# Kernel tuning notes

Hardware: AMD Instinct MI355X
Metric: run time of the kernel (lower is better)

## Reference

```python
import jax, jax.numpy as jnp
import numpy as np

B, LAT, NF, IMG, N_CALLS = 8, 512, 64, 128, 4
N_LAYERS = int(np.ceil(np.log2(IMG) - np.log2(16))) + 1  # 4 resolutions: 16,32,64,128
CF = 3  # SinSobel perception factor: identity + sobel_x + sobel_y
FIN, FH, FOUT = NF * CF, NF, NF * 2  # gated => 2*n_filter out of dyna block
P_SIZES = [FH * FIN, FH, FOUT * FH, FOUT, FOUT * FIN, FOUT]
P_OFFS = np.cumsum([0] + P_SIZES)
P_TOT = int(P_OFFS[-1])

_g1 = np.exp(-0.5 * np.array([-1.0, 0.0, 1.0]) ** 2)
_gk = np.outer(_g1, _g1); _gk = _gk / _gk.sum()
GAUSS_K = jnp.asarray(_gk, jnp.float32)
SOBEL_X = jnp.asarray(np.array([[-1, 0, 1], [-2, 0, 2], [-1, 0, 1]], np.float32) / 8.0)
SOBEL_Y = SOBEL_X.T


def _dwconv3(x, k):
    # depthwise 3x3 conv, 'same' padding; x: [B,C,H,W], k: [3,3]
    C = x.shape[1]
    kern = jnp.broadcast_to(k[None, None], (C, 1, 3, 3)).astype(x.dtype)
    return jax.lax.conv_general_dilated(
        x, kern, (1, 1), ((1, 1), (1, 1)),
        dimension_numbers=('NCHW', 'OIHW', 'NCHW'), feature_group_count=C)


def sin_sobel(x):
    # perception: [x, sobel_x(x), sobel_y(x)] -> 3*C channels
    return jnp.concatenate([x, _dwconv3(x, SOBEL_X), _dwconv3(x, SOBEL_Y)], axis=1)


def inst_norm(x, eps=1e-5):
    m = x.mean((2, 3), keepdims=True)
    v = x.var((2, 3), keepdims=True)
    return (x - m) * jax.lax.rsqrt(v + eps)


def up2_blur(x, gk):
    b, c, h, w = x.shape
    x = jax.image.resize(x, (b, c, 2 * h, 2 * w), 'bilinear')  # align_corners=False
    return _dwconv3(x, gk)


def dyna_block(x, lat, hyper_w, hyper_b):
    # hypernetwork generates per-sample 1x1-conv residual block weights
    p = lat @ hyper_w + hyper_b  # [B, P_TOT]
    w1 = p[:, P_OFFS[0]:P_OFFS[1]].reshape(-1, FH, FIN)
    b1 = p[:, P_OFFS[1]:P_OFFS[2]]
    w2 = p[:, P_OFFS[2]:P_OFFS[3]].reshape(-1, FOUT, FH)
    b2 = p[:, P_OFFS[3]:P_OFFS[4]]
    ws = p[:, P_OFFS[4]:P_OFFS[5]].reshape(-1, FOUT, FIN)
    bs = p[:, P_OFFS[5]:P_OFFS[6]]
    h = jax.nn.relu(jnp.einsum('bihw,boi->bohw', x, w1) + b1[:, :, None, None])
    y = jnp.einsum('bihw,boi->bohw', h, w2) + b2[:, :, None, None]
    s = jnp.einsum('bihw,boi->bohw', x, ws) + bs[:, :, None, None]
    return s + y


def setup_inputs() -> dict:
    key = jax.random.key(0)
    ks = jax.random.split(key, 8)
    return dict(
        lat=jax.random.normal(ks[0], (B, LAT), jnp.float32),
        ca_noise=jax.random.normal(ks[1], (B, NF, 16, 16), jnp.float32),
        seed=jax.random.normal(ks[2], (1, NF, 1, 1), jnp.float32),  # spatially constant seed
        leak_factor=jnp.asarray(0.1, jnp.float32),
        hyper_w=jax.random.normal(ks[3], (LAT, P_TOT), jnp.float32) * 0.02,
        hyper_b=jnp.zeros((P_TOT,), jnp.float32),
        res1_w=jax.random.normal(ks[4], (NF, NF), jnp.float32) / np.sqrt(NF).astype(np.float32),
        res1_b=jnp.zeros((NF,), jnp.float32),
        res2_w=jax.random.normal(ks[5], (NF, NF), jnp.float32) / np.sqrt(NF).astype(np.float32),
        res2_b=jnp.zeros((NF,), jnp.float32),
        outc_w=jax.random.normal(ks[6], (3, NF), jnp.float32) / np.sqrt(NF).astype(np.float32),
        outc_b=jnp.zeros((3,), jnp.float32),
    )


def reference(lat, ca_noise, seed, leak_factor, hyper_w, hyper_b,
              res1_w, res1_b, res2_w, res2_b, outc_w, outc_b):
    # seed init branch: constant seed -> instance_norm -> 0, plus blurred ca_noise
    out = inst_norm(jnp.broadcast_to(seed, (B, NF, 16, 16)))
    out = out + _dwconv3(ca_noise, GAUSS_K)  # in_ds (resize 16->16 is identity)
    lf = jnp.clip(leak_factor, 0.001, 1000.0)
    for c in range(N_LAYERS * N_CALLS):
        z = sin_sobel(out)
        z = inst_norm(z)
        z = dyna_block(z, lat, hyper_w, hyper_b)
        z, g = jnp.split(z, 2, axis=1)  # gated
        z = z * jax.nn.sigmoid(g)
        out = out + lf * z
        if c < N_LAYERS * N_CALLS - 1 and c % N_CALLS == N_CALLS - 1:
            out = up2_blur(out, GAUSS_K)
    # out_conv: resize to IMG is identity here; 1x1 residual block + 1x1 conv
    h = jax.nn.relu(jnp.einsum('bihw,oi->bohw', out, res1_w) + res1_b[None, :, None, None])
    r = jnp.einsum('bihw,oi->bohw', h, res2_w) + res2_b[None, :, None, None]
    y = jnp.einsum('bihw,oi->bohw', out + r, outc_w) + outc_b[None, :, None, None]
    out_raw = y
    return jnp.clip(y, -1.0, 1.0), out_raw
```

## Files before the change

kernel.cpp:

```cpp
#include <hip/hip_runtime.h>
#include <math.h>

#define B 8
#define LATD 512
#define PT 45376
#define FIN 192
#define FH 64
#define OW1 0
#define OB1 12288
#define OW2 12352
#define OB2 20544
#define OWS 20672
#define OBS 45248
#define TPX 128
#define KC 16

__device__ __forceinline__ float gk_at(int ky, int kx){
  const float a = 0.60653065971263342f;
  const float inv = 1.0f / ((1.0f + 2.0f*a) * (1.0f + 2.0f*a));
  float wy = (ky==1) ? 1.0f : a;
  float wx = (kx==1) ? 1.0f : a;
  return wy * wx * inv;
}

__global__ void k_hyper(const float* __restrict__ lat, const float* __restrict__ hw,
                        const float* __restrict__ hb, float* __restrict__ p){
  __shared__ float slat[B*LATD];
  for (int idx = threadIdx.x; idx < B*LATD; idx += 256) slat[idx] = lat[idx];
  __syncthreads();
  int j = blockIdx.x*256 + threadIdx.x;
  if (j >= PT) return;
  float acc[B];
#pragma unroll
  for (int b=0;b<B;++b) acc[b]=0.f;
  for (int k=0;k<LATD;++k){
    float w = hw[(size_t)k*PT + j];
#pragma unroll
    for (int b=0;b<B;++b) acc[b] = fmaf(slat[b*LATD+k], w, acc[b]);
  }
  float bias = hb[j];
#pragma unroll
  for (int b=0;b<B;++b) p[(size_t)b*PT + j] = acc[b] + bias;
}

__global__ void k_init(const float* __restrict__ noise, float* __restrict__ out){
  int bc = blockIdx.x;
  int t = threadIdx.x;
  int y = t >> 4, x = t & 15;
  const float* src = noise + (size_t)bc*256;
  float acc = 0.f;
#pragma unroll
  for (int ky=0;ky<3;++ky){
    int yy = y+ky-1; if (yy < 0 || yy > 15) continue;
#pragma unroll
    for (int kx=0;kx<3;++kx){
      int xx = x+kx-1; if (xx < 0 || xx > 15) continue;
      acc = fmaf(gk_at(ky,kx), src[yy*16+xx], acc);
    }
  }
  out[(size_t)bc*256 + t] = acc;
}

__global__ void __launch_bounds__(256) k_sobstat(const float* __restrict__ out, float* __restrict__ sob,
                    float* __restrict__ stats, int H, int lgH, int HW){
  int bc = blockIdx.x; int b = bc >> 6, c = bc & 63;
  int t = threadIdx.x;
  const float* src = out + ((size_t)(b*64+c))*(size_t)HW;
  float* dxp = sob + ((size_t)(b*128 + c))*(size_t)HW;
  float* dyp = sob + ((size_t)(b*128 + 64 + c))*(size_t)HW;
  float s0=0.f,q0=0.f,sx=0.f,qx=0.f,sy=0.f,qy=0.f;
  for (int px = t*4; px < HW; px += 1024){
    int y = px >> lgH, x = px & (H-1);
    float rm[6], rc[6], rp[6];
    float4 v = *(const float4*)(src + px);
    rc[1]=v.x; rc[2]=v.y; rc[3]=v.z; rc[4]=v.w;
    rc[0] = (x>0)     ? src[px-1] : 0.f;
    rc[5] = (x+4 < H) ? src[px+4] : 0.f;
    s0 += v.x+v.y+v.z+v.w;
    q0 += v.x*v.x+v.y*v.y+v.z*v.z+v.w*v.w;
    if (y > 0){
      const float* r = src + px - H;
      float4 u = *(const float4*)r;
      rm[1]=u.x; rm[2]=u.y; rm[3]=u.z; rm[4]=u.w;
      rm[0] = (x>0)     ? r[-1] : 0.f;
      rm[5] = (x+4 < H) ? r[4]  : 0.f;
    } else { rm[0]=rm[1]=rm[2]=rm[3]=rm[4]=rm[5]=0.f; }
    if (y+1 < H){
      const float* r = src + px + H;
      float4 u = *(const float4*)r;
      rp[1]=u.x; rp[2]=u.y; rp[3]=u.z; rp[4]=u.w;
      rp[0] = (x>0)     ? r[-1] : 0.f;
      rp[5] = (x+4 < H) ? r[4]  : 0.f;
    } else { rp[0]=rp[1]=rp[2]=rp[3]=rp[4]=rp[5]=0.f; }
    float dxv[4], dyv[4];
#pragma unroll
    for (int j=0;j<4;++j){
      dxv[j] = ((rm[j+2]-rm[j]) + 2.f*(rc[j+2]-rc[j]) + (rp[j+2]-rp[j])) * 0.125f;
      dyv[j] = ((rp[j] + 2.f*rp[j+1] + rp[j+2]) - (rm[j] + 2.f*rm[j+1] + rm[j+2])) * 0.125f;
      sx += dxv[j]; qx = fmaf(dxv[j],dxv[j],qx);
      sy += dyv[j]; qy = fmaf(dyv[j],dyv[j],qy);
    }
    float4 o1; o1.x=dxv[0]; o1.y=dxv[1]; o1.z=dxv[2]; o1.w=dxv[3];
    float4 o2; o2.x=dyv[0]; o2.y=dyv[1]; o2.z=dyv[2]; o2.w=dyv[3];
    *(float4*)(dxp + px) = o1;
    *(float4*)(dyp + px) = o2;
  }
  float vals[6] = {s0,q0,sx,qx,sy,qy};
  __shared__ float rbuf[6][4];
  int lane = t & 63, wid = t >> 6;
#pragma unroll
  for (int i=0;i<6;++i){
    float v = vals[i];
#pragma unroll
    for (int off=32; off; off>>=1) v += __shfl_down(v, off, 64);
    if (lane==0) rbuf[i][wid] = v;
  }
  __syncthreads();
  if (t < 3){
    float s = rbuf[t*2][0]+rbuf[t*2][1]+rbuf[t*2][2]+rbuf[t*2][3];
    float q = rbuf[t*2+1][0]+rbuf[t*2+1][1]+rbuf[t*2+1][2]+rbuf[t*2+1][3];
    float inv = 1.0f/(float)HW;
    float m = s*inv;
    float var = fmaxf(q*inv - m*m, 0.f);
    float r = 1.0f/sqrtf(var + 1e-5f);
    int ch = b*192 + c + t*64;
    stats[ch*2]   = -m*r;
    stats[ch*2+1] = r;
  }
}

__device__ __forceinline__ float4 ldx(const float* __restrict__ out, const float* __restrict__ sob,
                                      const float* __restrict__ stats,
                                      int b, int i, int off, int HW){
  const float* src = (i < 64) ? out + ((size_t)(b*64+i))*(size_t)HW
                              : sob + ((size_t)(b*128+(i-64)))*(size_t)HW;
  float4 v = *(const float4*)(src + off);
  float c = stats[(b*192+i)*2], r = stats[(b*192+i)*2+1];
  v.x = fmaf(v.x, r, c); v.y = fmaf(v.y, r, c);
  v.z = fmaf(v.z, r, c); v.w = fmaf(v.w, r, c);
  return v;
}

#define XS(k,p)  bufA[(k)*128 + (p)]
#define W1S(k,o) bufA[2048 + (k)*68 + (o)]
#define HS(k,p)  bufA[(k)*128 + (p)]
#define WZS(k,o) bufB[(k)*128 + (o)]
__global__ void __launch_bounds__(256, 3) k_dyna(float* __restrict__ out, const float* __restrict__ sob,
                       const float* __restrict__ stats, const float* __restrict__ p,
                       const float* __restrict__ lfp, int HW){
  __shared__ float bufA[8192];
  __shared__ float bufB[2048];
  int b = blockIdx.y;
  int tx = threadIdx.x, ty = threadIdx.y;
  int tid = ty*16 + tx;
  int px0 = blockIdx.x*TPX;
  const float* pw = p + (size_t)b*PT;

  float az[4][8], ag[4][8], ah[4][8];
#pragma unroll
  for (int k=0;k<4;++k)
#pragma unroll
    for (int j=0;j<8;++j){ az[k][j]=0.f; ag[k][j]=0.f; ah[k][j]=0.f; }

  const int xch0 = tid>>5,        xc4 = tid&31;
  const int xch1 = 8 + (tid>>5);
  const int wo0  = tid>>2,        wk  = tid&3;
  const int wo1  = 64 + (tid>>2);

  float4 vx0, vx1, vz0, vz1, v10;

  vx0 = ldx(out, sob, stats, b, xch0, px0 + xc4*4, HW);
  vx1 = ldx(out, sob, stats, b, xch1, px0 + xc4*4, HW);
  vz0 = *(const float4*)(pw + OWS + wo0*FIN + wk*4);
  vz1 = *(const float4*)(pw + OWS + wo1*FIN + wk*4);
  v10 = *(const float4*)(pw + OW1 + wo0*FIN + wk*4);

  for (int ci=0; ci<12; ++ci){
    __syncthreads();
    *(float4*)(&XS(xch0, xc4*4)) = vx0;
    *(float4*)(&XS(xch1, xc4*4)) = vx1;
    WZS(wk*4+0,wo0)=vz0.x; WZS(wk*4+1,wo0)=vz0.y; WZS(wk*4+2,wo0)=vz0.z; WZS(wk*4+3,wo0)=vz0.w;
    WZS(wk*4+0,wo1)=vz1.x; WZS(wk*4+1,wo1)=vz1.y; WZS(wk*4+2,wo1)=vz1.z; WZS(wk*4+3,wo1)=vz1.w;
    W1S(wk*4+0,wo0)=v10.x; W1S(wk*4+1,wo0)=v10.y; W1S(wk*4+2,wo0)=v10.z; W1S(wk*4+3,wo0)=v10.w;
    if (ci+1 < 12){
      int cn = ci+1;
      vx0 = ldx(out, sob, stats, b, cn*KC+xch0, px0 + xc4*4, HW);
      vx1 = ldx(out, sob, stats, b, cn*KC+xch1, px0 + xc4*4, HW);
      vz0 = *(const float4*)(pw + OWS + wo0*FIN + cn*KC + wk*4);
      vz1 = *(const float4*)(pw + OWS + wo1*FIN + cn*KC + wk*4);
      v10 = *(const float4*)(pw + OW1 + wo0*FIN + cn*KC + wk*4);
    }
    __syncthreads();
#pragma unroll 4
    for (int kk=0; kk<KC; ++kk){
      float4 xa = *(const float4*)(&XS(kk, tx*4));
      float4 xb = *(const float4*)(&XS(kk, (tx+16)*4));
      float4 wz4 = *(const float4*)(&WZS(kk, ty*4));
      float4 wg4 = *(const float4*)(&WZS(kk, 64+ty*4));
      float4 w14 = *(const float4*)(&W1S(kk, ty*4));
      float xv[8] = {xa.x,xa.y,xa.z,xa.w,xb.x,xb.y,xb.z,xb.w};
      float wzv[4]= {wz4.x,wz4.y,wz4.z,wz4.w};
      float wgv[4]= {wg4.x,wg4.y,wg4.z,wg4.w};
      float w1v[4]= {w14.x,w14.y,w14.z,w14.w};
#pragma unroll
      for (int k=0;k<4;++k)
#pragma unroll
        for (int j=0;j<8;++j){
          az[k][j] = fmaf(wzv[k], xv[j], az[k][j]);
          ag[k][j] = fmaf(wgv[k], xv[j], ag[k][j]);
          ah[k][j] = fmaf(w1v[k], xv[j], ah[k][j]);
        }
    }
  }

  vz0 = *(const float4*)(pw + OW2 + wo0*FH + wk*4);
  vz1 = *(const float4*)(pw + OW2 + wo1*FH + wk*4);

  __syncthreads();

#pragma unroll
  for (int k=0;k<4;++k){
    float b1 = pw[OB1 + ty*4 + k];
#pragma unroll
    for (int h=0; h<2; ++h){
      float4 r;
      r.x = fmaxf(ah[k][h*4+0]+b1, 0.f);
      r.y = fmaxf(ah[k][h*4+1]+b1, 0.f);
      r.z = fmaxf(ah[k][h*4+2]+b1, 0.f);
      r.w = fmaxf(ah[k][h*4+3]+b1, 0.f);
      *(float4*)(&HS(ty*4+k, (tx+h*16)*4)) = r;
    }
  }

  for (int ci=0; ci<4; ++ci){
    __syncthreads();
    WZS(wk*4+0,wo0)=vz0.x; WZS(wk*4+1,wo0)=vz0.y; WZS(wk*4+2,wo0)=vz0.z; WZS(wk*4+3,wo0)=vz0.w;
    WZS(wk*4+0,wo1)=vz1.x; WZS(wk*4+1,wo1)=vz1.y; WZS(wk*4+2,wo1)=vz1.z; WZS(wk*4+3,wo1)=vz1.w;
    if (ci+1 < 4){
      int cn = ci+1;
      vz0 = *(const float4*)(pw + OW2 + wo0*FH + cn*KC + wk*4);
      vz1 = *(const float4*)(pw + OW2 + wo1*FH + cn*KC + wk*4);
    }
    __syncthreads();
#pragma unroll 4
    for (int kk=0; kk<KC; ++kk){
      float4 xa = *(const float4*)(&HS(ci*KC+kk, tx*4));
      float4 xb = *(const float4*)(&HS(ci*KC+kk, (tx+16)*4));
      float4 wz4 = *(const float4*)(&WZS(kk, ty*4));
      float4 wg4 = *(const float4*)(&WZS(kk, 64+ty*4));
      float xv[8] = {xa.x,xa.y,xa.z,xa.w,xb.x,xb.y,xb.z,xb.w};
      float wzv[4]= {wz4.x,wz4.y,wz4.z,wz4.w};
      float wgv[4]= {wg4.x,wg4.y,wg4.z,wg4.w};
#pragma unroll
      for (int k=0;k<4;++k)
#pragma unroll
        for (int j=0;j<8;++j){
          az[k][j] = fmaf(wzv[k], xv[j], az[k][j]);
          ag[k][j] = fmaf(wgv[k], xv[j], ag[k][j]);
        }
    }
  }

  float lf = fminf(fmaxf(lfp[0], 0.001f), 1000.f);
#pragma unroll
  for (int k=0;k<4;++k){
    int o = ty*4 + k;
    float bz = pw[OB2 + o]      + pw[OBS + o];
    float bg = pw[OB2 + o + 64] + pw[OBS + o + 64];
    float* op = out + ((size_t)(b*64+o))*(size_t)HW + px0;
#pragma unroll
    for (int h=0; h<2; ++h){
      float4 ov = *(const float4*)(op + (tx + h*16)*4);
      float r[4];
#pragma unroll
      for (int j=0;j<4;++j){
        float z = az[k][h*4+j] + bz;
        float g = ag[k][h*4+j] + bg;
        r[j] = lf * z / (1.f + expf(-g));
      }
      ov.x += r[0]; ov.y += r[1]; ov.z += r[2]; ov.w += r[3];
      *(float4*)(op + (tx + h*16)*4) = ov;
    }
  }
}

__global__ void k_upsample(const float* __restrict__ src, float* __restrict__ dst, int H, int lgH){
  int Hn = 2*H;
  int HWn = Hn*Hn;
  int bc = blockIdx.y;
  int o4 = (blockIdx.x*256 + threadIdx.x)*4;
  const float* s = src + (size_t)bc*(size_t)(H*H);
  int oy = o4 >> (lgH+1), ox0 = o4 & (Hn-1);
  int m = ox0 >> 1;
  int xm1 = (m-1 < 0)   ? 0   : m-1;
  int xp1 = (m+1 > H-1) ? H-1 : m+1;
  int xp2 = (m+2 > H-1) ? H-1 : m+2;
  float u[3][6];
#pragma unroll
  for (int ky=0; ky<3; ++ky){
    int yy = oy + ky - 1;
    if (yy < 0 || yy >= Hn){
#pragma unroll
      for (int j=0;j<6;++j) u[ky][j] = 0.f;
      continue;
    }
    int iy = yy >> 1, ry = yy & 1;
    int y0 = ry ? iy : iy-1;
    int y1 = ry ? iy+1 : iy;
    float wy0 = ry ? 0.75f : 0.25f;
    float wy1 = 1.f - wy0;
    y0 = y0 < 0 ? 0 : y0;
    y1 = y1 > H-1 ? H-1 : y1;
    const float* r0 = s + y0*H;
    const float* r1 = s + y1*H;
    float sv0 = wy0*r0[xm1] + wy1*r1[xm1];
    float sv1 = wy0*r0[m]   + wy1*r1[m];
    float sv2 = wy0*r0[xp1] + wy1*r1[xp1];
    float sv3 = wy0*r0[xp2] + wy1*r1[xp2];
    u[ky][0] = 0.75f*sv0 + 0.25f*sv1;
    u[ky][1] = 0.25f*sv0 + 0.75f*sv1;
    u[ky][2] = 0.75f*sv1 + 0.25f*sv2;
    u[ky][3] = 0.25f*sv1 + 0.75f*sv2;
    u[ky][4] = 0.75f*sv2 + 0.25f*sv3;
    u[ky][5] = 0.25f*sv2 + 0.75f*sv3;
    if (ox0 == 0)       u[ky][0] = 0.f;
    if (ox0 + 4 == Hn)  u[ky][5] = 0.f;
  }
  float res[4];
#pragma unroll
  for (int jo=0; jo<4; ++jo){
    float a = 0.f;
#pragma unroll
    for (int ky=0; ky<3; ++ky){
      a = fmaf(gk_at(ky,0), u[ky][jo],   a);
      a = fmaf(gk_at(ky,1), u[ky][jo+1], a);
      a = fmaf(gk_at(ky,2), u[ky][jo+2], a);
    }
    res[jo] = a;
  }
  float4 o; o.x=res[0]; o.y=res[1]; o.z=res[2]; o.w=res[3];
  *(float4*)(dst + (size_t)bc*(size_t)HWn + o4) = o;
}

__global__ void __launch_bounds__(256) k_final(const float* __restrict__ t,
    const float* __restrict__ r1w, const float* __restrict__ r1b,
    const float* __restrict__ r2w, const float* __restrict__ r2b,
    const float* __restrict__ ocw, const float* __restrict__ ocb,
    float* __restrict__ dout, int HW){
  __shared__ float Ts[64][132];
  __shared__ float Hs[64][132];
  __shared__ float Wb[64][68];
  int b = blockIdx.y;
  int tx = threadIdx.x, ty = threadIdx.y;
  int tid = ty*16 + tx;
  int px0 = blockIdx.x*TPX;

#pragma unroll
  for (int it=0; it<8; ++it){
    int idx = it*256 + tid;
    int ch = idx>>5, c4 = idx&31;
    *(float4*)(&Ts[ch][c4*4]) = *(const float4*)(t + ((size_t)(b*64+ch))*(size_t)HW + px0 + c4*4);
  }
#pragma unroll
  for (int it=0; it<4; ++it){
    int idx = it*256 + tid;
    int o = idx>>4, k4 = idx&15;
    float4 w = *(const float4*)(r1w + o*64 + k4*4);
    Wb[k4*4+0][o]=w.x; Wb[k4*4+1][o]=w.y; Wb[k4*4+2][o]=w.z; Wb[k4*4+3][o]=w.w;
  }
  __syncthreads();

  float acc[4][8];
#pragma unroll
  for (int k=0;k<4;++k)
#pragma unroll
    for (int j=0;j<8;++j) acc[k][j]=0.f;
#pragma unroll 4
  for (int kk=0; kk<64; ++kk){
    float4 xa = *(const float4*)(&Ts[kk][tx*4]);
    float4 xb = *(const float4*)(&Ts[kk][(tx+16)*4]);
    float4 w4 = *(const float4*)(&Wb[kk][ty*4]);
    float xv[8]={xa.x,xa.y,xa.z,xa.w,xb.x,xb.y,xb.z,xb.w};
    float wv[4]={w4.x,w4.y,w4.z,w4.w};
#pragma unroll
    for (int k=0;k<4;++k)
#pragma unroll
      for (int j=0;j<8;++j) acc[k][j] = fmaf(wv[k], xv[j], acc[k][j]);
  }
  __syncthreads();

#pragma unroll
  for (int k=0;k<4;++k){
    float bs = r1b[ty*4+k];
#pragma unroll
    for (int h=0; h<2; ++h){
      float4 r;
      r.x = fmaxf(acc[k][h*4+0]+bs, 0.f);
      r.y = fmaxf(acc[k][h*4+1]+bs, 0.f);
      r.z = fmaxf(acc[k][h*4+2]+bs, 0.f);
      r.w = fmaxf(acc[k][h*4+3]+bs, 0.f);
      *(float4*)(&Hs[ty*4+k][(tx+h*16)*4]) = r;
    }
  }
#pragma unroll
  for (int it=0; it<4; ++it){
    int idx = it*256 + tid;
    int o = idx>>4, k4 = idx&15;
    float4 w = *(const float4*)(r2w + o*64 + k4*4);
    Wb[k4*4+0][o]=w.x; Wb[k4*4+1][o]=w.y; Wb[k4*4+2][o]=w.z; Wb[k4*4+3][o]=w.w;
  }
  __syncthreads();

#pragma unroll
  for (int k=0;k<4;++k)
#pragma unroll
    for (int j=0;j<8;++j) acc[k][j]=0.f;
#pragma unroll 4
  for (int kk=0; kk<64; ++kk){
    float4 xa = *(const float4*)(&Hs[kk][tx*4]);
    float4 xb = *(const float4*)(&Hs[kk][(tx+16)*4]);
    float4 w4 = *(const float4*)(&Wb[kk][ty*4]);
    float xv[8]={xa.x,xa.y,xa.z,xa.w,xb.x,xb.y,xb.z,xb.w};
    float wv[4]={w4.x,w4.y,w4.z,w4.w};
#pragma unroll
    for (int k=0;k<4;++k)
#pragma unroll
      for (int j=0;j<8;++j) acc[k][j] = fmaf(wv[k], xv[j], acc[k][j]);
  }
#pragma unroll
  for (int k=0;k<4;++k){
    int o = ty*4 + k;
    float bs = r2b[o];
#pragma unroll
    for (int h=0; h<2; ++h){
      float4 tv = *(const float4*)(&Ts[o][(tx+h*16)*4]);
      tv.x += acc[k][h*4+0]+bs; tv.y += acc[k][h*4+1]+bs;
      tv.z += acc[k][h*4+2]+bs; tv.w += acc[k][h*4+3]+bs;
      *(float4*)(&Ts[o][(tx+h*16)*4]) = tv;
    }
  }
  __syncthreads();
  if (tid < 192){
    int c = tid>>6, kk = tid&63;
    Wb[kk][c] = ocw[c*64+kk];
  }
  __syncthreads();

  if (tid < 128){
    float a0=0.f, a1=0.f, a2=0.f;
#pragma unroll 4
    for (int kk=0; kk<64; ++kk){
      float x = Ts[kk][tid];
      a0 = fmaf(x, Wb[kk][0], a0);
      a1 = fmaf(x, Wb[kk][1], a1);
      a2 = fmaf(x, Wb[kk][2], a2);
    }
    size_t rawoff = (size_t)B*3*(size_t)HW;
    float y[3] = {a0+ocb[0], a1+ocb[1], a2+ocb[2]};
    int px = px0 + tid;
#pragma unroll
    for (int c=0;c<3;++c){
      size_t base = ((size_t)(b*3+c))*(size_t)HW + px;
      dout[base] = fminf(fmaxf(y[c],-1.f),1.f);
      dout[rawoff + base] = y[c];
    }
  }
}

extern "C" void kernel_launch(void* const* d_in, const int* in_sizes, int n_in,
                              void* d_out, int out_size, void* d_ws, size_t ws_size,
                              hipStream_t stream) {
  const float* lat = (const float*)d_in[0];
  const float* ca  = (const float*)d_in[1];
  const float* lfp = (const float*)d_in[3];
  const float* hw  = (const float*)d_in[4];
  const float* hb  = (const float*)d_in[5];
  const float* r1w = (const float*)d_in[6];
  const float* r1b = (const float*)d_in[7];
  const float* r2w = (const float*)d_in[8];
  const float* r2b = (const float*)d_in[9];
  const float* ocw = (const float*)d_in[10];
  const float* ocb = (const float*)d_in[11];
  float* dout = (float*)d_out;

  float* ws   = (float*)d_ws;
  float* p    = ws;
  float* outA = p    + (size_t)B*PT;
  float* outB = outA + (size_t)B*64*16384;
  float* sob  = outB + (size_t)B*64*16384;
  float* stats= sob  + (size_t)B*128*16384;

  k_hyper<<<dim3((PT+255)/256), dim3(256), 0, stream>>>(lat, hw, hb, p);
  k_init<<<dim3(B*64), dim3(256), 0, stream>>>(ca, outA);

  float* cur = outA;
  float* oth = outB;
  int H = 16, lgH = 4;
  for (int c = 0; c < 16; ++c){
    int HW = H*H;
    k_sobstat<<<dim3(B*64), dim3(256), 0, stream>>>(cur, sob, stats, H, lgH, HW);
    k_dyna<<<dim3(HW/TPX, B), dim3(16,16), 0, stream>>>(cur, sob, stats, p, lfp, HW);
    if (c < 15 && (c & 3) == 3){
      k_upsample<<<dim3((HW*4)/1024, B*64), dim3(256), 0, stream>>>(cur, oth, H, lgH);
      float* tmp = cur; cur = oth; oth = tmp;
      H *= 2; lgH += 1;
    }
  }
  int HW = H*H;
  k_final<<<dim3(HW/TPX, B), dim3(16,16), 0, stream>>>(cur, r1w, r1b, r2w, r2b, ocw, ocb, dout, HW);
}
```

Measured before the change: 1.534 ms.

## Double-buffer dyna LDS tiles and use narrower pixel tiles at low resolutions

Makes k_dyna a template over pixels-per-thread. It double-buffers the X and weight tiles in shared memory, which cuts one barrier per K-chunk and overlaps global loads with compute. Resolutions below 128 launch 64-pixel tiles so the 16/32/64 grids get twice as many blocks. Costs are a larger shared-memory footprint per block and smaller per-thread work, which lowers register reuse at small sizes.

```diff
diff --git a/kernel.cpp b/kernel.cpp
--- a/kernel.cpp
+++ b/kernel.cpp
@@ -12,7 +12,6 @@
 #define OB2 20544
 #define OWS 20672
 #define OBS 45248
-#define TPX 128
 #define KC 16
 
 __device__ __forceinline__ float gk_at(int ky, int kx){
@@ -141,124 +140,156 @@
   return v;
 }
 
-#define XS(k,p)  bufA[(k)*128 + (p)]
-#define W1S(k,o) bufA[2048 + (k)*68 + (o)]
-#define HS(k,p)  bufA[(k)*128 + (p)]
-#define WZS(k,o) bufB[(k)*128 + (o)]
+template<int PPT>
 __global__ void __launch_bounds__(256, 3) k_dyna(float* __restrict__ out, const float* __restrict__ sob,
                        const float* __restrict__ stats, const float* __restrict__ p,
                        const float* __restrict__ lfp, int HW){
-  __shared__ float bufA[8192];
-  __shared__ float bufB[2048];
+  constexpr int TPXT  = 16*PPT;
+  constexpr int XST   = TPXT + 4;
+  constexpr int XHALF = KC*XST;
+  constexpr int W1OFF = 2*XHALF;
+  constexpr int W1HALF= KC*68;
+  constexpr int HSZ   = 64*XST;
+  constexpr int ASZ   = (W1OFF + 2*W1HALF > HSZ) ? (W1OFF + 2*W1HALF) : HSZ;
+  __shared__ float bufA[ASZ];
+  __shared__ float bufB[2*KC*132];
+
   int b = blockIdx.y;
   int tx = threadIdx.x, ty = threadIdx.y;
   int tid = ty*16 + tx;
-  int px0 = blockIdx.x*TPX;
+  int px0 = blockIdx.x*TPXT;
   const float* pw = p + (size_t)b*PT;
 
-  float az[4][8], ag[4][8], ah[4][8];
+  float az[4][PPT], ag[4][PPT], ah[4][PPT];
 #pragma unroll
   for (int k=0;k<4;++k)
 #pragma unroll
-    for (int j=0;j<8;++j){ az[k][j]=0.f; ag[k][j]=0.f; ah[k][j]=0.f; }
-
-  const int xch0 = tid>>5,        xc4 = tid&31;
-  const int xch1 = 8 + (tid>>5);
-  const int wo0  = tid>>2,        wk  = tid&3;
-  const int wo1  = 64 + (tid>>2);
+    for (int j=0;j<PPT;++j){ az[k][j]=0.f; ag[k][j]=0.f; ah[k][j]=0.f; }
+
+  const int wo0 = tid>>2, wk = tid&3, wo1 = 64 + wo0;
 
   float4 vx0, vx1, vz0, vz1, v10;
 
-  vx0 = ldx(out, sob, stats, b, xch0, px0 + xc4*4, HW);
-  vx1 = ldx(out, sob, stats, b, xch1, px0 + xc4*4, HW);
-  vz0 = *(const float4*)(pw + OWS + wo0*FIN + wk*4);
-  vz1 = *(const float4*)(pw + OWS + wo1*FIN + wk*4);
-  v10 = *(const float4*)(pw + OW1 + wo0*FIN + wk*4);
-
-  for (int ci=0; ci<12; ++ci){
-    __syncthreads();
-    *(float4*)(&XS(xch0, xc4*4)) = vx0;
-    *(float4*)(&XS(xch1, xc4*4)) = vx1;
-    WZS(wk*4+0,wo0)=vz0.x; WZS(wk*4+1,wo0)=vz0.y; WZS(wk*4+2,wo0)=vz0.z; WZS(wk*4+3,wo0)=vz0.w;
-    WZS(wk*4+0,wo1)=vz1.x; WZS(wk*4+1,wo1)=vz1.y; WZS(wk*4+2,wo1)=vz1.z; WZS(wk*4+3,wo1)=vz1.w;
-    W1S(wk*4+0,wo0)=v10.x; W1S(wk*4+1,wo0)=v10.y; W1S(wk*4+2,wo0)=v10.z; W1S(wk*4+3,wo0)=v10.w;
-    if (ci+1 < 12){
-      int cn = ci+1;
-      vx0 = ldx(out, sob, stats, b, cn*KC+xch0, px0 + xc4*4, HW);
-      vx1 = ldx(out, sob, stats, b, cn*KC+xch1, px0 + xc4*4, HW);
-      vz0 = *(const float4*)(pw + OWS + wo0*FIN + cn*KC + wk*4);
-      vz1 = *(const float4*)(pw + OWS + wo1*FIN + cn*KC + wk*4);
-      v10 = *(const float4*)(pw + OW1 + wo0*FIN + cn*KC + wk*4);
-    }
-    __syncthreads();
+  auto loadX = [&](int ci){
+    if constexpr (PPT==8){
+      vx0 = ldx(out,sob,stats,b, ci*KC + (tid>>5),     px0 + (tid&31)*4, HW);
+      vx1 = ldx(out,sob,stats,b, ci*KC + 8 + (tid>>5), px0 + (tid&31)*4, HW);
+    } else {
+      vx0 = ldx(out,sob,stats,b, ci*KC + (tid>>4),     px0 + (tid&15)*4, HW);
+    }
+  };
+  auto loadW1z = [&](int ci){
+    vz0 = *(const float4*)(pw + OWS + wo0*FIN + ci*KC + wk*4);
+    vz1 = *(const float4*)(pw + OWS + wo1*FIN + ci*KC + wk*4);
+    v10 = *(const float4*)(pw + OW1 + wo0*FIN + ci*KC + wk*4);
+  };
+  auto loadW2 = [&](int ci){
+    vz0 = *(const float4*)(pw + OW2 + wo0*FH + ci*KC + wk*4);
+    vz1 = *(const float4*)(pw + OW2 + wo1*FH + ci*KC + wk*4);
+  };
+  auto writeX = [&](int bf){
+    if constexpr (PPT==8){
+      *(float4*)(&bufA[bf*XHALF + (tid>>5)*XST     + (tid&31)*4]) = vx0;
+      *(float4*)(&bufA[bf*XHALF + ((tid>>5)+8)*XST + (tid&31)*4]) = vx1;
+    } else {
+      *(float4*)(&bufA[bf*XHALF + (tid>>4)*XST     + (tid&15)*4]) = vx0;
+    }
+  };
+  auto writeWz = [&](int bf){
+    float* WZ = &bufB[bf*(KC*132)];
+    WZ[(wk*4+0)*132+wo0]=vz0.x; WZ[(wk*4+1)*132+wo0]=vz0.y; WZ[(wk*4+2)*132+wo0]=vz0.z; WZ[(wk*4+3)*132+wo0]=vz0.w;
+    WZ[(wk*4+0)*132+wo1]=vz1.x; WZ[(wk*4+1)*132+wo1]=vz1.y; WZ[(wk*4+2)*132+wo1]=vz1.z; WZ[(wk*4+3)*132+wo1]=vz1.w;
+  };
+  auto writeW1 = [&](int bf){
+    float* W1 = &bufA[W1OFF + bf*W1HALF];
+    W1[(wk*4+0)*68+wo0]=v10.x; W1[(wk*4+1)*68+wo0]=v10.y; W1[(wk*4+2)*68+wo0]=v10.z; W1[(wk*4+3)*68+wo0]=v10.w;
+  };
+  auto computeA = [&](int bf){
 #pragma unroll 4
     for (int kk=0; kk<KC; ++kk){
-      float4 xa = *(const float4*)(&XS(kk, tx*4));
-      float4 xb = *(const float4*)(&XS(kk, (tx+16)*4));
-      float4 wz4 = *(const float4*)(&WZS(kk, ty*4));
-      float4 wg4 = *(const float4*)(&WZS(kk, 64+ty*4));
-      float4 w14 = *(const float4*)(&W1S(kk, ty*4));
-      float xv[8] = {xa.x,xa.y,xa.z,xa.w,xb.x,xb.y,xb.z,xb.w};
-      float wzv[4]= {wz4.x,wz4.y,wz4.z,wz4.w};
-      float wgv[4]= {wg4.x,wg4.y,wg4.z,wg4.w};
-      float w1v[4]= {w14.x,w14.y,w14.z,w14.w};
+      float4 xa  = *(const float4*)(&bufA[bf*XHALF + kk*XST + tx*4]);
+      float4 wz4 = *(const float4*)(&bufB[bf*(KC*132) + kk*132 + ty*4]);
+      float4 wg4 = *(const float4*)(&bufB[bf*(KC*132) + kk*132 + 64 + ty*4]);
+      float4 w14 = *(const float4*)(&bufA[W1OFF + bf*W1HALF + kk*68 + ty*4]);
+      float xv[PPT];
+      xv[0]=xa.x; xv[1]=xa.y; xv[2]=xa.z; xv[3]=xa.w;
+      if constexpr (PPT==8){
+        float4 xb = *(const float4*)(&bufA[bf*XHALF + kk*XST + (tx+16)*4]);
+        xv[4]=xb.x; xv[5]=xb.y; xv[6]=xb.z; xv[7]=xb.w;
+      }
+      float wzv[4]={wz4.x,wz4.y,wz4.z,wz4.w};
+      float wgv[4]={wg4.x,wg4.y,wg4.z,wg4.w};
+      float w1v[4]={w14.x,w14.y,w14.z,w14.w};
 #pragma unroll
       for (int k=0;k<4;++k)
 #pragma unroll
-        for (int j=0;j<8;++j){
+        for (int j=0;j<PPT;++j){
           az[k][j] = fmaf(wzv[k], xv[j], az[k][j]);
           ag[k][j] = fmaf(wgv[k], xv[j], ag[k][j]);
           ah[k][j] = fmaf(w1v[k], xv[j], ah[k][j]);
         }
     }
-  }
-
-  vz0 = *(const float4*)(pw + OW2 + wo0*FH + wk*4);
-  vz1 = *(const float4*)(pw + OW2 + wo1*FH + wk*4);
-
-  __syncthreads();
+  };
+  auto computeC = [&](int ci, int bf){
+#pragma unroll 4
+    for (int kk=0; kk<KC; ++kk){
+      float4 xa  = *(const float4*)(&bufA[(ci*KC+kk)*XST + tx*4]);
+      float4 wz4 = *(const float4*)(&bufB[bf*(KC*132) + kk*132 + ty*4]);
+      float4 wg4 = *(const float4*)(&bufB[bf*(KC*132) + kk*132 + 64 + ty*4]);
+      float xv[PPT];
+      xv[0]=xa.x; xv[1]=xa.y; xv[2]=xa.z; xv[3]=xa.w;
+      if constexpr (PPT==8){
+        float4 xb = *(const float4*)(&bufA[(ci*KC+kk)*XST + (tx+16)*4]);
+        xv[4]=xb.x; xv[5]=xb.y; xv[6]=xb.z; xv[7]=xb.w;
+      }
+      float wzv[4]={wz4.x,wz4.y,wz4.z,wz4.w};
+      float wgv[4]={wg4.x,wg4.y,wg4.z,wg4.w};
+#pragma unroll
+      for (int k=0;k<4;++k)
+#pragma unroll
+        for (int j=0;j<PPT;++j){
+          az[k][j] = fmaf(wzv[k], xv[j], az[k][j]);
+          ag[k][j] = fmaf(wgv[k], xv[j], ag[k][j]);
+        }
+    }
+  };
+
+  loadX(0); loadW1z(0);
+  writeX(0); writeWz(0); writeW1(0);
+  loadX(1); loadW1z(1);
+  __syncthreads();
+  for (int ci=0; ci<12; ++ci){
+    int cur = ci & 1;
+    if (ci < 11){ writeX(cur^1); writeWz(cur^1); writeW1(cur^1); }
+    if (ci < 10){ loadX(ci+2); loadW1z(ci+2); }
+    else if (ci == 10){ loadW2(0); }
+    computeA(cur);
+    __syncthreads();
+  }
 
 #pragma unroll
   for (int k=0;k<4;++k){
     float b1 = pw[OB1 + ty*4 + k];
 #pragma unroll
-    for (int h=0; h<2; ++h){
+    for (int h=0; h<PPT/4; ++h){
       float4 r;
       r.x = fmaxf(ah[k][h*4+0]+b1, 0.f);
       r.y = fmaxf(ah[k][h*4+1]+b1, 0.f);
       r.z = fmaxf(ah[k][h*4+2]+b1, 0.f);
       r.w = fmaxf(ah[k][h*4+3]+b1, 0.f);
-      *(float4*)(&HS(ty*4+k, (tx+h*16)*4)) = r;
-    }
-  }
+      *(float4*)(&bufA[(ty*4+k)*XST + (tx+h*16)*4]) = r;
+    }
+  }
+  writeWz(0);
+  loadW2(1);
+  __syncthreads();
 
   for (int ci=0; ci<4; ++ci){
+    int cur = ci & 1;
+    if (ci < 3) writeWz(cur^1);
+    if (ci < 2) loadW2(ci+2);
+    computeC(ci, cur);
     __syncthreads();
-    WZS(wk*4+0,wo0)=vz0.x; WZS(wk*4+1,wo0)=vz0.y; WZS(wk*4+2,wo0)=vz0.z; WZS(wk*4+3,wo0)=vz0.w;
-    WZS(wk*4+0,wo1)=vz1.x; WZS(wk*4+1,wo1)=vz1.y; WZS(wk*4+2,wo1)=vz1.z; WZS(wk*4+3,wo1)=vz1.w;
-    if (ci+1 < 4){
-      int cn = ci+1;
-      vz0 = *(const float4*)(pw + OW2 + wo0*FH + cn*KC + wk*4);
-      vz1 = *(const float4*)(pw + OW2 + wo1*FH + cn*KC + wk*4);
-    }
-    __syncthreads();
-#pragma unroll 4
-    for (int kk=0; kk<KC; ++kk){
-      float4 xa = *(const float4*)(&HS(ci*KC+kk, tx*4));
-      float4 xb = *(const float4*)(&HS(ci*KC+kk, (tx+16)*4));
-      float4 wz4 = *(const float4*)(&WZS(kk, ty*4));
-      float4 wg4 = *(const float4*)(&WZS(kk, 64+ty*4));
-      float xv[8] = {xa.x,xa.y,xa.z,xa.w,xb.x,xb.y,xb.z,xb.w};
-      float wzv[4]= {wz4.x,wz4.y,wz4.z,wz4.w};
-      float wgv[4]= {wg4.x,wg4.y,wg4.z,wg4.w};
-#pragma unroll
-      for (int k=0;k<4;++k)
-#pragma unroll
-        for (int j=0;j<8;++j){
-          az[k][j] = fmaf(wzv[k], xv[j], az[k][j]);
-          ag[k][j] = fmaf(wgv[k], xv[j], ag[k][j]);
-        }
-    }
   }
 
   float lf = fminf(fmaxf(lfp[0], 0.001f), 1000.f);
@@ -269,7 +300,7 @@
     float bg = pw[OB2 + o + 64] + pw[OBS + o + 64];
     float* op = out + ((size_t)(b*64+o))*(size_t)HW + px0;
 #pragma unroll
-    for (int h=0; h<2; ++h){
+    for (int h=0; h<PPT/4; ++h){
       float4 ov = *(const float4*)(op + (tx + h*16)*4);
       float r[4];
 #pragma unroll
@@ -353,7 +384,7 @@
   int b = blockIdx.y;
   int tx = threadIdx.x, ty = threadIdx.y;
   int tid = ty*16 + tx;
-  int px0 = blockIdx.x*TPX;
+  int px0 = blockIdx.x*128;
 
 #pragma unroll
   for (int it=0; it<8; ++it){
@@ -499,7 +530,10 @@
   for (int c = 0; c < 16; ++c){
     int HW = H*H;
     k_sobstat<<<dim3(B*64), dim3(256), 0, stream>>>(cur, sob, stats, H, lgH, HW);
-    k_dyna<<<dim3(HW/TPX, B), dim3(16,16), 0, stream>>>(cur, sob, stats, p, lfp, HW);
+    if (H >= 128)
+      k_dyna<8><<<dim3(HW/128, B), dim3(16,16), 0, stream>>>(cur, sob, stats, p, lfp, HW);
+    else
+      k_dyna<4><<<dim3(HW/64,  B), dim3(16,16), 0, stream>>>(cur, sob, stats, p, lfp, HW);
     if (c < 15 && (c & 3) == 3){
       k_upsample<<<dim3((HW*4)/1024, B*64), dim3(256), 0, stream>>>(cur, oth, H, lgH);
       float* tmp = cur; cur = oth; oth = tmp;
@@ -507,5 +541,5 @@
     }
   }
   int HW = H*H;
-  k_final<<<dim3(HW/TPX, B), dim3(16,16), 0, stream>>>(cur, r1w, r1b, r2w, r2b, ocw, ocb, dout, HW);
-}
+  k_final<<<dim3(HW/128, B), dim3(16,16), 0, stream>>>(cur, r1w, r1b, r2w, r2b, ocw, ocb, dout, HW);
+}
```

New measurement: 1.350 ms. -12.0%, faster.
